# Kernel optimization log

Measured on AMD Instinct MI355X. Metric: run time of the kernel, lower is better.

The kernel has to match this reference:

```python
import jax, jax.numpy as jnp
import numpy as np

NUM_CLASSES = 80
IMG = 640
STRIDES = (8, 16, 32)
CENTER_RADIUS = 2.5
TOPK = 10  # n_candidate_k; dynamic_ks = clamp(int(sum top-10 IoU), 1) <= 10


def _make_grids():
    gs, ss = [], []
    for s in STRIDES:
        n = IMG // s
        gy, gx = np.meshgrid(np.arange(n), np.arange(n), indexing="ij")
        gs.append(np.stack([gx.ravel(), gy.ravel()], 1).astype(np.float32))
        ss.append(np.full(n * n, s, np.float32))
    return np.concatenate(gs, 0), np.concatenate(ss, 0)


def setup_inputs() -> dict:
    key = jax.random.key(0)
    B, T, C = 16, 128, NUM_CLASSES
    grid_np, stride_np = _make_grids()
    A = grid_np.shape[0]  # 8400
    k1, k2, k3, k4, k5, k6 = jax.random.split(key, 6)
    # pred boxes: plausible abs xyxy around anchor centers
    ctr = jnp.asarray((grid_np + 0.5) * stride_np[:, None])[None]
    ctr = ctr + 4.0 * jax.random.normal(k1, (B, A, 2))
    wh = jnp.asarray(stride_np)[None, :, None] * jax.random.uniform(k2, (B, A, 2), minval=1.0, maxval=4.0)
    box = jnp.concatenate([ctr - wh / 2, ctr + wh / 2], -1)
    logits = 2.0 * jax.random.normal(k3, (B, A, 1 + C))
    pred = jnp.concatenate([box, logits], -1)  # [B, A, 5+C]
    # targets: [B, T, 6] = (batch_id, cid, x1, y1, x2, y2)
    tc = jax.random.uniform(k4, (B, T, 2), minval=60.0, maxval=580.0)
    twh = jax.random.uniform(k5, (B, T, 2), minval=30.0, maxval=200.0)
    tbox = jnp.concatenate([tc - twh / 2, tc + twh / 2], -1)
    cid = jax.random.randint(k6, (B, T, 1), 0, C).astype(jnp.float32)
    bid = jnp.broadcast_to(jnp.arange(B, dtype=jnp.float32)[:, None, None], (B, T, 1))
    target = jnp.concatenate([bid, cid, tbox], -1)
    return {"pred": pred, "target": target,
            "grid_mask": jnp.asarray(grid_np), "stride_mask": jnp.asarray(stride_np)}


def _pairwise_iou(a, b):
    # a [T,4], b [A,4], xyxy -> [T,A]
    lt = jnp.maximum(a[:, None, :2], b[None, :, :2])
    rb = jnp.minimum(a[:, None, 2:], b[None, :, 2:])
    wh = jnp.clip(rb - lt, 0.0, None)
    inter = wh[..., 0] * wh[..., 1]
    area_a = jnp.clip(a[:, 2] - a[:, 0], 0.0, None) * jnp.clip(a[:, 3] - a[:, 1], 0.0, None)
    area_b = jnp.clip(b[:, 2] - b[:, 0], 0.0, None) * jnp.clip(b[:, 3] - b[:, 1], 0.0, None)
    return inter / (area_a[:, None] + area_b[None, :] - inter + 1e-8)


def _ciou(p, t):
    # complete IoU, elementwise over leading dims, xyxy
    lt = jnp.maximum(p[..., :2], t[..., :2])
    rb = jnp.minimum(p[..., 2:], t[..., 2:])
    wh = jnp.clip(rb - lt, 0.0, None)
    inter = wh[..., 0] * wh[..., 1]
    wp, hp = p[..., 2] - p[..., 0], p[..., 3] - p[..., 1]
    wt, ht = t[..., 2] - t[..., 0], t[..., 3] - t[..., 1]
    iou = inter / (wp * hp + wt * ht - inter + 1e-8)
    cwh = jnp.maximum(p[..., 2:], t[..., 2:]) - jnp.minimum(p[..., :2], t[..., :2])
    c2 = cwh[..., 0] ** 2 + cwh[..., 1] ** 2 + 1e-8
    rho2 = (((p[..., 0] + p[..., 2]) - (t[..., 0] + t[..., 2])) ** 2
            + ((p[..., 1] + p[..., 3]) - (t[..., 1] + t[..., 3])) ** 2) / 4.0
    v = (4.0 / jnp.pi ** 2) * (jnp.arctan(wt / (ht + 1e-8)) - jnp.arctan(wp / (hp + 1e-8))) ** 2
    alpha = v / (1.0 - iou + v + 1e-8)
    return iou - rho2 / c2 - alpha * v


def _bce_logits(x, t):
    return jnp.maximum(x, 0.0) - x * t + jnp.log1p(jnp.exp(-jnp.abs(x)))


def _assign_image(pred_i, tgt_i, grid, stride):
    # pred_i [A,5+C], tgt_i [T,6]
    A, T, C = pred_i.shape[0], tgt_i.shape[0], NUM_CLASSES
    tbox = tgt_i[:, 2:6]
    cid = tgt_i[:, 1].astype(jnp.int32)
    xc = (grid[:, 0] + 0.5) * stride  # [A]
    yc = (grid[:, 1] + 0.5) * stride
    d = jnp.stack([xc[None] - tbox[:, 0:1], yc[None] - tbox[:, 1:2],
                   tbox[:, 2:3] - xc[None], tbox[:, 3:4] - yc[None]], -1)  # [T,A,4]
    in_boxes = d.min(-1) > 0.0  # [T,A]
    txc = (tbox[:, 0] + tbox[:, 2]) / 2
    tyc = (tbox[:, 1] + tbox[:, 3]) / 2
    in_centers = jnp.maximum(jnp.abs(xc[None] - txc[:, None]),
                             jnp.abs(yc[None] - tyc[:, None])) < CENTER_RADIUS * stride[None]
    in_box = in_boxes.any(0) | in_centers.any(0)  # [A], candidate anchors
    in_box_center = in_boxes & in_centers  # [T,A]
    iou = jnp.where(in_box[None], _pairwise_iou(tbox, pred_i[:, :4]), 0.0)  # [T,A]
    iou_cost = -jnp.log(iou + 1e-8)
    prob = jnp.sqrt(jax.nn.sigmoid(pred_i[:, 4:5]) * jax.nn.sigmoid(pred_i[:, 5:]))  # [A,C]
    logp = jnp.maximum(jnp.log(prob), -100.0)      # torch BCE clamps log at -100
    log1mp = jnp.maximum(jnp.log1p(-prob), -100.0)
    # sum_c BCE(prob, onehot(cid)) computed analytically (avoids [T,A,C]):
    cls_cost = -(log1mp.sum(-1)[None, :] + (logp - log1mp)[:, cid].T)  # [T,A]
    # 1e9 keeps anchors outside in_box out of the candidate pool (original slices them away)
    cost = cls_cost + 3.0 * iou_cost + 1e5 * (~in_box_center) + 1e9 * (~in_box)[None, :]
    topk_ious, _ = jax.lax.top_k(iou, TOPK)  # [T,10]
    dyn_k = jnp.maximum(topk_ious.sum(1).astype(jnp.int32), 1)  # [T]
    _, idx = jax.lax.top_k(-cost, TOPK)  # 10 lowest-cost anchors per target
    sel = jnp.arange(TOPK)[None, :] < dyn_k[:, None]  # keep first dyn_k of them
    matching = jnp.zeros((T, A), bool).at[jnp.arange(T)[:, None], idx].set(sel)
    matching = matching & in_box[None, :]
    conflict = matching.sum(0) > 1  # anchors claimed by >1 targets
    keep = jnp.arange(T)[:, None] == jnp.argmin(cost, 0)[None, :]  # [T,A]
    matching = jnp.where(conflict[None, :], keep, matching)
    mp = matching.any(0)  # [A]
    tp = jnp.argmax(matching, 0)  # [A] target index per anchor
    p_iou = jnp.clip((iou / (iou.max(1, keepdims=True) + 1e-8)).max(0), 0.0, 1.0)  # [A]
    obj_t = jnp.where(in_box, p_iou, 0.0)
    box_t = tbox[tp]  # [A,4]
    cls_t = jax.nn.one_hot(cid[tp], C, dtype=jnp.float32)  # [A,C]
    return mp, box_t, obj_t, cls_t


def reference(pred, target, grid_mask, stride_mask):
    B, A = pred.shape[:2]
    C = NUM_CLASSES
    mp, box_t, obj_t, cls_t = jax.lax.stop_gradient(
        jax.vmap(_assign_image, in_axes=(0, 0, None, None))(pred, target, grid_mask, stride_mask))
    m = mp.reshape(-1).astype(pred.dtype)  # matched-anchor mask over B*A
    n = jnp.maximum(m.sum(), 1.0)
    p = pred.reshape(B * A, -1)
    lbox = 0.05 * jnp.sum((1.0 - _ciou(p[:, :4], box_t.reshape(-1, 4))) * m) / n
    lobj = _bce_logits(p[:, 4], obj_t.reshape(-1)).mean()
    lcls = 0.5 * jnp.sum(_bce_logits(p[:, 5:], cls_t.reshape(-1, C)).mean(-1) * m) / n
    loss = lbox + lobj + lcls
    return loss, jnp.stack([lbox, lobj, lcls])
```

## Files before the change

### kernel.cpp

```cpp
#include <hip/hip_runtime.h>
#include <cfloat>

#pragma clang fp contract(off)

#define NCLS 80
#define PDIM 85
#define NA   8400
#define NAP  8448
#define NB   16
#define NT   128
#define NTOP 10
#define APB  64
#define BPI  132
#define BPI2 33
#define LN2  0.6931471805599453f
#define CAPW 512

#define BAPC ((size_t)NB*NAP)

#define KSENT 0xFFFFFFFF7FFFFFFFull

__device__ __forceinline__ float bce_fast(float x, float t){
  float ax = fabsf(x);
  float e  = __expf(-ax);
  return fmaxf(x,0.0f) - x*t + LN2*__builtin_amdgcn_logf(1.0f + e);
}

__device__ __forceinline__ float pair_iou(float tx1,float ty1,float tx2,float ty2,
                                          float px1,float py1,float px2,float py2){
  float w = fminf(tx2,px2) - fmaxf(tx1,px1);
  float h = fminf(ty2,py2) - fmaxf(ty1,py1);
  w = fmaxf(w,0.0f); h = fmaxf(h,0.0f);
  float inter = w*h;
  float at = fmaxf(tx2-tx1,0.0f)*fmaxf(ty2-ty1,0.0f);
  float ap = fmaxf(px2-px1,0.0f)*fmaxf(py2-py1,0.0f);
  float den = at+ap-inter+1e-8f;
  return inter * __builtin_amdgcn_rcpf(den);
}

__device__ __forceinline__ float dval_exact(float ol, float lg){
  float e4 = __expf(-fabsf(ol));
  float L4 = LN2*__builtin_amdgcn_logf(1.0f + e4);
  float ln_sobj = -(fmaxf(-ol,0.0f) + L4);
  float e  = __expf(-fabsf(lg));
  float L  = LN2*__builtin_amdgcn_logf(1.0f + e);
  float ln_sc = -(fmaxf(-lg,0.0f) + L);
  float lph = 0.5f*(ln_sobj + ln_sc);
  float p   = __expf(lph);
  float lp  = fmaxf(lph, -100.0f);
  float l1  = fmaxf(LN2*__builtin_amdgcn_logf(fmaxf(1.0f - p, 0.0f)), -100.0f);
  return lp - l1;
}

__device__ __forceinline__ float cost_from(float S, float dval, float iou, bool ibc, bool ib){
  float iouc = -LN2 * __builtin_amdgcn_logf(iou + 1e-8f);
  float clsc = -(S + dval);
  float c = clsc + 3.0f*iouc;
  c = c + (ibc ? 0.0f : 100000.0f);
  c = c + (ib  ? 0.0f : 1000000000.0f);
  return c;
}

__device__ __forceinline__ unsigned long long key_of(float c, int idx){
  unsigned int u = __float_as_uint(c);
  u ^= (u & 0x80000000u) ? 0xFFFFFFFFu : 0x80000000u;
  return ((unsigned long long)u << 32) | (unsigned int)idx;
}

__device__ __forceinline__ void ins_iou(float* riou, float iou){
  if (iou > riou[NTOP-1]){
    #pragma unroll
    for (int j = NTOP-1; j >= 1; --j){
      bool gj  = iou > riou[j];
      bool gj1 = iou > riou[j-1];
      riou[j] = gj ? (gj1 ? riou[j-1] : iou) : riou[j];
    }
    riou[0] = (iou > riou[0]) ? iou : riou[0];
  }
}
__device__ __forceinline__ void ins_key(unsigned long long* rk, unsigned long long key){
  if (key < rk[NTOP-1]){
    #pragma unroll
    for (int j = NTOP-1; j >= 1; --j){
      bool bj  = key < rk[j];
      bool bj1 = key < rk[j-1];
      rk[j] = bj ? (bj1 ? rk[j-1] : key) : rk[j];
    }
    rk[0] = (key < rk[0]) ? key : rk[0];
  }
}

__global__ __launch_bounds__(256) void k0_precompute(
    const float* __restrict__ pred, const float* __restrict__ target,
    const float* __restrict__ grid, const float* __restrict__ stridev,
    float4* __restrict__ pbox4, float4* __restrict__ meta4,
    float* __restrict__ obja, float* __restrict__ S0a,
    unsigned long long* __restrict__ mask, unsigned int* __restrict__ obju,
    float4* __restrict__ gaabb, unsigned long long* __restrict__ actm,
    float* __restrict__ acc)
{
  __shared__ __align__(16) float tile[APB*PDIM];
  __shared__ float4 tb4s[NT];
  __shared__ float  ps_s[4][APB];
  __shared__ float  ps0_s[4][APB];
  __shared__ int    ib_s[4][APB];

  int i  = blockIdx.x / BPI;
  int b  = blockIdx.x % BPI;
  int c0 = b*APB;
  int n  = NA - c0; if (n > APB) n = APB;
  int tid = threadIdx.x;

  if (blockIdx.x == 0) acc[tid] = 0.0f;

  const float4* src4 = (const float4*)(pred + ((size_t)i*NA + c0)*PDIM);
  int tot4 = (n*PDIM) >> 2;
  for (int idx = tid; idx < tot4; idx += 256) ((float4*)tile)[idx] = src4[idx];
  for (int idx = tid; idx < NT; idx += 256){
    const float* tg = target + (i*NT + idx)*6;
    tb4s[idx] = make_float4(tg[2],tg[3],tg[4],tg[5]);
  }
  __syncthreads();

  int al = tid & 63, cg = tid >> 6;
  if (al < n){
    float x4 = tile[al*PDIM+4];
    float e4 = __expf(-fabsf(x4));
    float L4 = LN2*__builtin_amdgcn_logf(1.0f + e4);
    float ln_sobj = -(fmaxf(-x4,0.0f) + L4);
    float ps = 0.0f, ps0 = 0.0f;
    #pragma unroll 4
    for (int k = 0; k < 20; ++k){
      int c = cg*20 + k;
      float x  = tile[al*PDIM+5+c];
      float e  = __expf(-fabsf(x));
      float L  = LN2*__builtin_amdgcn_logf(1.0f + e);
      float ln_sc = -(fmaxf(-x,0.0f) + L);
      float lph = 0.5f*(ln_sobj + ln_sc);
      float p   = __expf(lph);
      float l1  = fmaxf(LN2*__builtin_amdgcn_logf(fmaxf(1.0f - p, 0.0f)), -100.0f);
      ps  += l1;
      ps0 += fmaxf(x,0.0f) + L;
    }
    ps_s[cg][al] = ps; ps0_s[cg][al] = ps0;

    int ga = c0 + al;
    float xg = grid[2*ga], yg = grid[2*ga+1], sv = stridev[ga];
    float xc = (xg + 0.5f)*sv, yc = (yg + 0.5f)*sv;
    float rc = 2.5f*sv;
    bool ibp = false;
    #pragma unroll 4
    for (int t = cg*32; t < cg*32+32; ++t){
      float4 T = tb4s[t];
      bool inb = (xc-T.x>0.0f)&&(yc-T.y>0.0f)&&(T.z-xc>0.0f)&&(T.w-yc>0.0f);
      float txc=(T.x+T.z)*0.5f, tyc=(T.y+T.w)*0.5f;
      bool inc = fmaxf(fabsf(xc-txc),fabsf(yc-tyc)) < rc;
      ibp = ibp || inb || inc;
    }
    ib_s[cg][al] = ibp ? 1 : 0;
  }
  __syncthreads();

  if (tid < APB){
    int a = tid;
    bool real = (a < n);
    int gid = i*NAP + c0 + a;
    float x1=0,y1=0,x2=0,y2=0,xc=0,yc=0,rc=0;
    bool ib = false;

    if (real){
      float s  = ps_s[0][a]  + ps_s[1][a]  + ps_s[2][a]  + ps_s[3][a];
      float s0 = ps0_s[0][a] + ps0_s[1][a] + ps0_s[2][a] + ps0_s[3][a];
      ib  = (ib_s[0][a] | ib_s[1][a] | ib_s[2][a] | ib_s[3][a]) != 0;

      x1 = tile[a*PDIM+0]; y1 = tile[a*PDIM+1];
      x2 = tile[a*PDIM+2]; y2 = tile[a*PDIM+3];
      float ol = tile[a*PDIM+4];
      pbox4[gid] = make_float4(x1,y1,x2,y2);
      obja[gid]  = ol;
      S0a[gid]   = s0;
      mask[(size_t)gid*2]   = 0ull;
      mask[(size_t)gid*2+1] = 0ull;
      obju[gid] = 0u;

      int ga = c0 + a;
      float xg = grid[2*ga], yg = grid[2*ga+1], sv = stridev[ga];
      xc = (xg + 0.5f)*sv; yc = (yg + 0.5f)*sv;
      rc = 2.5f*sv;
      meta4[gid] = make_float4(xc, yc, ib ? rc : -rc, s);
    } else {
      meta4[gid] = make_float4(0.0f, 0.0f, -1.0f, 0.0f);
      pbox4[gid] = make_float4(0.0f, 0.0f, 0.0f, 0.0f);
      obju[gid]  = 0u;
    }

    bool iv = real && ib;
    unsigned long long am = __ballot(iv);
    float bx1 = iv ? x1 : FLT_MAX,  by1 = iv ? y1 : FLT_MAX;
    float bx2 = iv ? x2 : -FLT_MAX, by2 = iv ? y2 : -FLT_MAX;
    float cx1 = iv ? xc : FLT_MAX,  cy1 = iv ? yc : FLT_MAX;
    float cx2 = iv ? xc : -FLT_MAX, cy2 = iv ? yc : -FLT_MAX;
    float rx1 = iv ? xc-rc : FLT_MAX,  ry1 = iv ? yc-rc : FLT_MAX;
    float rx2 = iv ? xc+rc : -FLT_MAX, ry2 = iv ? yc+rc : -FLT_MAX;
    #pragma unroll
    for (int off = 32; off > 0; off >>= 1){
      bx1 = fminf(bx1, __shfl_xor(bx1, off));
      by1 = fminf(by1, __shfl_xor(by1, off));
      bx2 = fmaxf(bx2, __shfl_xor(bx2, off));
      by2 = fmaxf(by2, __shfl_xor(by2, off));
      cx1 = fminf(cx1, __shfl_xor(cx1, off));
      cy1 = fminf(cy1, __shfl_xor(cy1, off));
      cx2 = fmaxf(cx2, __shfl_xor(cx2, off));
      cy2 = fmaxf(cy2, __shfl_xor(cy2, off));
      rx1 = fminf(rx1, __shfl_xor(rx1, off));
      ry1 = fminf(ry1, __shfl_xor(ry1, off));
      rx2 = fmaxf(rx2, __shfl_xor(rx2, off));
      ry2 = fmaxf(ry2, __shfl_xor(ry2, off));
    }
    if (tid == 0){
      size_t gb = (size_t)(i*BPI + b)*3;
      gaabb[gb+0] = make_float4(bx1,by1,bx2,by2);
      gaabb[gb+1] = make_float4(cx1,cy1,cx2,cy2);
      gaabb[gb+2] = make_float4(rx1,ry1,rx2,ry2);
      actm[i*BPI + b] = am;
    }
  }
}

__global__ __launch_bounds__(256) void k1_pertarget(
    const float4* __restrict__ pbox4, const float4* __restrict__ meta4,
    const float* __restrict__ obja, const float* __restrict__ pred,
    const float* __restrict__ target, const float4* __restrict__ gaabb,
    const unsigned long long* __restrict__ actm,
    unsigned int* __restrict__ obju, unsigned long long* __restrict__ mask)
{
  __shared__ int2  seg2[4*CAPW];
  __shared__ int   cnts_s[4], cibc_s[4];
  __shared__ float wiou[4][NTOP];
  __shared__ unsigned long long wkey[4][NTOP];
  __shared__ float rmax_s;

  int tid = threadIdx.x, lane = tid & 63, w = tid >> 6;
  int g = blockIdx.x;
  int i = g / NT, t = g - i*NT;
  int iNAP = i*NAP;
  int iNA  = i*NA;
  const float* m4f = (const float*)meta4;

  const float* tg = target + (size_t)g*6;
  int   cid = (int)tg[1];
  float tx1 = tg[2], ty1 = tg[3], tx2 = tg[4], ty2 = tg[5];
  float txc = (tx1+tx2)*0.5f, tyc = (ty1+ty2)*0.5f;

  bool sv = false, svi = false;
  if (lane < 33){
    size_t gb = (size_t)(i*BPI + (w + 4*lane))*3;
    float4 gbb = gaabb[gb+0];
    float4 gcc = gaabb[gb+1];
    float4 grr = gaabb[gb+2];
    bool ovg  = (fminf(tx2,gbb.z) > fmaxf(tx1,gbb.x)) &&
                (fminf(ty2,gbb.w) > fmaxf(ty1,gbb.y));
    bool inbg = (gcc.z > tx1) && (gcc.x < tx2) && (gcc.w > ty1) && (gcc.y < ty2);
    bool incg = (txc > grr.x) && (txc < grr.z) && (tyc > grr.y) && (tyc < grr.w);
    svi = inbg && incg;
    sv = ovg || svi;
  }
  unsigned long long gmsk  = __ballot(sv);
  unsigned long long gmski = __ballot(svi);

  int cnt = 0, ci = 0;
  while (gmsk){
    int k = __ffsll(gmsk) - 1;
    unsigned long long kb = 1ull << k;
    gmsk &= gmsk - 1;
    int a = w*64 + k*256 + lane;
    float4 pb = pbox4[iNAP+a];

    bool ov  = (fminf(tx2,pb.z) > fmaxf(tx1,pb.x)) &&
               (fminf(ty2,pb.w) > fmaxf(ty1,pb.y));

    if (gmski & kb){
      float4 mt = meta4[iNAP+a];
      bool act = (mt.z > 0.0f);
      bool inb = (mt.x-tx1>0.0f)&&(mt.y-ty1>0.0f)&&(tx2-mt.x>0.0f)&&(ty2-mt.y>0.0f);
      bool inc = fmaxf(fabsf(mt.x-txc),fabsf(mt.y-tyc)) < mt.z;
      bool ibc = inb && inc;
      bool cand = act && (ov || ibc);
      unsigned long long bb  = __ballot(cand);
      unsigned long long bb2 = __ballot(ibc);
      if (cand){
        int pos = cnt + __popcll(bb & ((1ull << lane) - 1ull));
        if (pos < CAPW) seg2[w*CAPW + pos].x = a | (ibc ? (1<<15) : 0);
      }
      cnt += __popcll(bb);
      ci  += __popcll(bb2);
    } else {
      unsigned long long am = actm[i*BPI + (w + 4*k)];
      bool act = (am >> lane) & 1ull;
      bool cand = act && ov;
      unsigned long long bb = __ballot(cand);
      if (cand){
        int pos = cnt + __popcll(bb & ((1ull << lane) - 1ull));
        if (pos < CAPW) seg2[w*CAPW + pos].x = a;
      }
      cnt += __popcll(bb);
    }
  }
  if (lane == 0){ cnts_s[w] = cnt; cibc_s[w] = ci; }
  __syncthreads();

  int tibc = cibc_s[0]+cibc_s[1]+cibc_s[2]+cibc_s[3];
  bool ovf = (cnts_s[0]>CAPW)||(cnts_s[1]>CAPW)||(cnts_s[2]>CAPW)||(cnts_s[3]>CAPW);
  bool fastp = !ovf && (tibc >= 16);

  float riou[NTOP]; unsigned long long rk[NTOP];
  #pragma unroll
  for (int j=0;j<NTOP;++j){ riou[j]=0.0f; rk[j]=KSENT; }

  int cw = cnts_s[w];
  if (fastp){
    for (int j = lane; j < cw; j += 64){
      int e  = seg2[w*CAPW + j].x;
      int a1 = e & 0x3fff;
      bool ibc = (e & (1<<15)) != 0;
      int gid = iNAP + a1;
      float4 pb2 = pbox4[gid];
      float iou = pair_iou(tx1,ty1,tx2,ty2, pb2.x,pb2.y,pb2.z,pb2.w);
      seg2[w*CAPW + j].y = __float_as_int(iou);
      ins_iou(riou, iou);
      float S  = m4f[(size_t)gid*4 + 3];
      float dv = dval_exact(obja[gid], pred[(size_t)(iNA+a1)*PDIM + 5 + cid]);
      float c  = cost_from(S, dv, iou, ibc, true);
      ins_key(rk, key_of(c, a1));
    }
  } else {
    for (int a1 = tid; a1 < NA; a1 += 256){
      float4 mt2 = meta4[iNAP+a1];
      if (mt2.z > 0.0f){
        float4 pb2 = pbox4[iNAP+a1];
        float iou = pair_iou(tx1,ty1,tx2,ty2, pb2.x,pb2.y,pb2.z,pb2.w);
        ins_iou(riou, iou);
        bool inb = (mt2.x-tx1>0.0f)&&(mt2.y-ty1>0.0f)&&(tx2-mt2.x>0.0f)&&(ty2-mt2.y>0.0f);
        bool inc = fmaxf(fabsf(mt2.x-txc),fabsf(mt2.y-tyc)) < mt2.z;
        float dv = dval_exact(obja[iNAP+a1], pred[(size_t)(iNA+a1)*PDIM + 5 + cid]);
        float c = cost_from(mt2.w, dv, iou, inb&&inc, true);
        ins_key(rk, key_of(c, a1));
      }
    }
  }

  #pragma unroll
  for (int r = 0; r < NTOP; ++r){
    float gm = riou[0];
    #pragma unroll
    for (int m = 1; m < 64; m <<= 1) gm = fmaxf(gm, __shfl_xor(gm, m));
    unsigned long long bb = __ballot(riou[0] == gm);
    int win = __ffsll(bb) - 1;
    if (lane == win){
      #pragma unroll
      for (int j=0;j<NTOP-1;++j) riou[j] = riou[j+1];
      riou[NTOP-1] = 0.0f;
    }
    if (lane == 0) wiou[w][r] = gm;
  }
  #pragma unroll
  for (int r = 0; r < NTOP; ++r){
    unsigned long long gk = rk[0];
    #pragma unroll
    for (int m = 1; m < 64; m <<= 1){
      unsigned long long o = __shfl_xor(gk, m);
      gk = (o < gk) ? o : gk;
    }
    if (rk[0] == gk){
      #pragma unroll
      for (int j=0;j<NTOP-1;++j) rk[j] = rk[j+1];
      rk[NTOP-1] = KSENT;
    }
    if (lane == 0) wkey[w][r] = gk;
  }
  __syncthreads();

  int dk = 1;
  if (w == 0){
    int p0=0,p1=0,p2=0,p3=0;
    float ssum = 0.0f, rmax = 0.0f;
    #pragma unroll
    for (int r = 0; r < NTOP; ++r){
      float v0=wiou[0][p0], v1=wiou[1][p1], v2=wiou[2][p2], v3=wiou[3][p3];
      float mx = fmaxf(fmaxf(v0,v1), fmaxf(v2,v3));
      if (r == 0) rmax = mx;
      ssum += mx;
      if      (mx == v0) ++p0;
      else if (mx == v1) ++p1;
      else if (mx == v2) ++p2;
      else               ++p3;
    }
    dk = (int)ssum;
    if (dk < 1) dk = 1;
    if (lane == 0) rmax_s = rmax;
  }
  __syncthreads();

  float invm = 1.0f / (rmax_s + 1e-8f);
  if (fastp){
    for (int j = lane; j < cw; j += 64){
      int2 e = seg2[w*CAPW + j];
      int a1 = e.x & 0x3fff;
      float iou = __int_as_float(e.y);
      float v = iou * invm;
      if (v > 0.0f) atomicMax(&obju[iNAP + a1], __float_as_uint(v));
    }
  } else {
    for (int a1 = tid; a1 < NA; a1 += 256){
      float4 mt2 = meta4[iNAP+a1];
      if (mt2.z > 0.0f){
        float4 pb2 = pbox4[iNAP+a1];
        float iou = pair_iou(tx1,ty1,tx2,ty2, pb2.x,pb2.y,pb2.z,pb2.w);
        float v = iou * invm;
        if (v > 0.0f) atomicMax(&obju[iNAP+a1], __float_as_uint(v));
      }
    }
  }

  if (w == 0){
    int q0=0,q1=0,q2=0,q3=0;
    int myidx = 0x7fffffff;
    #pragma unroll
    for (int r = 0; r < NTOP; ++r){
      unsigned long long k0=wkey[0][q0], k1=wkey[1][q1], k2=wkey[2][q2], k3=wkey[3][q3];
      unsigned long long mn = k0;
      mn = (k1 < mn) ? k1 : mn;
      mn = (k2 < mn) ? k2 : mn;
      mn = (k3 < mn) ? k3 : mn;
      if (lane == r) myidx = (int)(mn & 0xFFFFFFFFull);
      if      (mn == k0) ++q0;
      else if (mn == k1) ++q1;
      else if (mn == k2) ++q2;
      else               ++q3;
    }

    if (lane < NTOP && lane < dk){
      int a1 = myidx;
      if (a1 >= 0 && a1 < NA){
        atomicOr(&mask[(size_t)(iNAP + a1)*2 + (t>>6)], 1ull << (t & 63));
      }
    }
  }
}

__global__ __launch_bounds__(256) void k2_peranchor(
    const float* __restrict__ pred,
    const float4* __restrict__ pbox4, const float4* __restrict__ meta4,
    const float* __restrict__ obja, const float* __restrict__ S0a,
    const float* __restrict__ target,
    const unsigned int* __restrict__ obju, const unsigned long long* __restrict__ mask,
    float* __restrict__ acc)
{
  __shared__ float4 tb4[NT];
  __shared__ int    tcid[NT];
  __shared__ int    cl[256];
  __shared__ int    bt_s[256];
  __shared__ int    ncl;
  __shared__ float4 part[4];

  int i  = blockIdx.x / BPI2;
  int b  = blockIdx.x - i*BPI2;
  int tid = threadIdx.x, lane = tid & 63, w = tid >> 6;
  int a  = b*256 + tid;
  int gid = i*NAP + a;

  if (tid < NT){
    const float* tg = target + (i*NT + tid)*6;
    tcid[tid] = (int)tg[1];
    tb4[tid]  = make_float4(tg[2],tg[3],tg[4],tg[5]);
  }
  if (tid == 0) ncl = 0;

  bool valid = (a < NA);
  float4 pb = pbox4[gid];
  float4 mt = meta4[gid];
  unsigned long long m0=0, m1=0;
  if (valid){ m0 = mask[(size_t)gid*2]; m1 = mask[(size_t)gid*2+1]; }
  float bestv = __uint_as_float(obju[gid]);
  float olv   = obja[gid];
  float S0v   = S0a[gid];

  bool ib = valid && (mt.z > 0.0f);
  float px1=pb.x, py1=pb.y, px2=pb.z, py2=pb.w;
  int cnt = __popcll(m0) + __popcll(m1);

  __syncthreads();

  bool myc = (cnt > 1);
  unsigned long long cb = __ballot(myc);
  int nb = __popcll(cb);
  int base = 0;
  if (lane == 0 && nb) base = atomicAdd(&ncl, nb);
  base = __shfl(base, 0);
  if (myc) cl[base + __popcll(cb & ((1ull << lane) - 1ull))] = tid;
  __syncthreads();

  int tot = ncl;
  for (int ci = w; ci < tot; ci += 4){
    int aidx = cl[ci];
    int a2g  = b*256 + aidx;
    int gid2 = i*NAP + a2g;
    float4 pb2 = pbox4[gid2];
    float4 mt2 = meta4[gid2];
    bool ib2 = (mt2.z > 0.0f);
    float rc2 = fabsf(mt2.z);
    float Sg  = mt2.w;
    float ol2 = obja[gid2];
    size_t pbase = (size_t)(i*NA + a2g)*PDIM;

    int ta = lane, tb = lane + 64;
    float dva = dval_exact(ol2, pred[pbase + 5 + tcid[ta]]);
    float dvb = dval_exact(ol2, pred[pbase + 5 + tcid[tb]]);

    float4 Ta = tb4[ta];
    float ioua = ib2 ? pair_iou(Ta.x,Ta.y,Ta.z,Ta.w,pb2.x,pb2.y,pb2.z,pb2.w) : 0.0f;
    bool inba = (mt2.x-Ta.x>0.0f)&&(mt2.y-Ta.y>0.0f)&&(Ta.z-mt2.x>0.0f)&&(Ta.w-mt2.y>0.0f);
    float txa=(Ta.x+Ta.z)*0.5f, tya=(Ta.y+Ta.w)*0.5f;
    bool inca = fmaxf(fabsf(mt2.x-txa),fabsf(mt2.y-tya)) < rc2;
    unsigned long long ka = key_of(cost_from(Sg, dva, ioua, inba&&inca, ib2), ta);

    float4 Tb = tb4[tb];
    float ioub = ib2 ? pair_iou(Tb.x,Tb.y,Tb.z,Tb.w,pb2.x,pb2.y,pb2.z,pb2.w) : 0.0f;
    bool inbb = (mt2.x-Tb.x>0.0f)&&(mt2.y-Tb.y>0.0f)&&(Tb.z-mt2.x>0.0f)&&(Tb.w-mt2.y>0.0f);
    float txb=(Tb.x+Tb.z)*0.5f, tyb=(Tb.y+Tb.w)*0.5f;
    bool incb = fmaxf(fabsf(mt2.x-txb),fabsf(mt2.y-tyb)) < rc2;
    unsigned long long kb = key_of(cost_from(Sg, dvb, ioub, inbb&&incb, ib2), tb);

    unsigned long long mn = (kb < ka) ? kb : ka;
    #pragma unroll
    for (int m = 1; m < 64; m <<= 1){
      unsigned long long o = __shfl_xor(mn, m);
      mn = (o < mn) ? o : mn;
    }
    if (lane == 0) bt_s[aidx] = (int)(mn & 0xFFFFFFFFull);
  }
  __syncthreads();

  float m=0.0f, vbox=0.0f, vobj=0.0f, vcls=0.0f;
  if (valid){
    float obj_t = ib ? fminf(fmaxf(bestv,0.0f),1.0f) : 0.0f;
    vobj = bce_fast(olv, obj_t);

    int tp = 0; bool mpv = false;
    if (cnt > 1){ tp = bt_s[tid]; mpv = true; }
    else if (cnt == 1){
      tp = m0 ? (__ffsll(m0)-1) : (64 + __ffsll(m1)-1);
      mpv = true;
    }

    if (mpv){
      m = 1.0f;
      float4 T = tb4[tp];
      float x1=T.x, y1=T.y, x2=T.z, y2=T.w;
      float w2 = fmaxf(fminf(px2,x2)-fmaxf(px1,x1),0.0f);
      float h2 = fmaxf(fminf(py2,y2)-fmaxf(py1,y1),0.0f);
      float inter = w2*h2;
      float wp=px2-px1, hp=py2-py1, wt=x2-x1, ht=y2-y1;
      float iou = inter/(wp*hp + wt*ht - inter + 1e-8f);
      float cw = fmaxf(px2,x2)-fminf(px1,x1);
      float ch = fmaxf(py2,y2)-fminf(py1,y1);
      float c2 = cw*cw + ch*ch + 1e-8f;
      float dx = (px1+px2)-(x1+x2), dy = (py1+py2)-(y1+y2);
      float rho2 = (dx*dx + dy*dy)/4.0f;
      float da = atanf(wt/(ht+1e-8f)) - atanf(wp/(hp+1e-8f));
      float v  = 0.4052847345693511f * da * da;
      float alpha = v/(1.0f - iou + v + 1e-8f);
      vbox = 1.0f - (iou - rho2/c2 - alpha*v);

      int cc = tcid[tp];
      float xcc = pred[(size_t)(i*NA + a)*PDIM + 5 + cc];
      vcls = (S0v - xcc) * (1.0f/80.0f);
    }
  }

  #pragma unroll
  for (int off=32; off>0; off>>=1){
    m    += __shfl_down(m, off);
    vbox += __shfl_down(vbox, off);
    vobj += __shfl_down(vobj, off);
    vcls += __shfl_down(vcls, off);
  }
  if (lane == 0) part[w] = make_float4(m, vbox, vobj, vcls);
  __syncthreads();
  if (tid == 0){
    float4 s0 = part[0], s1 = part[1], s2 = part[2], s3 = part[3];
    float4 s = make_float4(s0.x+s1.x+s2.x+s3.x, s0.y+s1.y+s2.y+s3.y,
                           s0.z+s1.z+s2.z+s3.z, s0.w+s1.w+s2.w+s3.w);
    int slot = (blockIdx.x & 63)*4;
    atomicAdd(&acc[slot+0], s.x);
    atomicAdd(&acc[slot+1], s.y);
    atomicAdd(&acc[slot+2], s.z);
    atomicAdd(&acc[slot+3], s.w);
  }
}

__global__ void k3_final(const float* __restrict__ acc, float* __restrict__ out){
  int l = threadIdx.x;
  float4 v = ((const float4*)acc)[l];
  #pragma unroll
  for (int off=32; off>0; off>>=1){
    v.x += __shfl_down(v.x, off);
    v.y += __shfl_down(v.y, off);
    v.z += __shfl_down(v.z, off);
    v.w += __shfl_down(v.w, off);
  }
  if (l == 0){
    float n    = fmaxf(v.x, 1.0f);
    float lbox = 0.05f * v.y / n;
    float lobj = v.z / (float)(NB*NA);
    float lcls = 0.5f  * v.w / n;
    out[0] = lbox + lobj + lcls;
    out[1] = lbox; out[2] = lobj; out[3] = lcls;
  }
}

extern "C" void kernel_launch(void* const* d_in, const int* in_sizes, int n_in,
                              void* d_out, int out_size, void* d_ws, size_t ws_size,
                              hipStream_t stream) {
  const float* pred    = (const float*)d_in[0];
  const float* target  = (const float*)d_in[1];
  const float* grid    = (const float*)d_in[2];
  const float* stridev = (const float*)d_in[3];
  float* out = (float*)d_out;

  char* ws = (char*)d_ws;

  size_t off = 0;
  unsigned long long* mask = (unsigned long long*)(ws + off); off += BAPC*16;
  float* acc    = (float*)(ws + off); off += 64*4*4;
  float4* pbox4 = (float4*)(ws + off); off += BAPC*16;
  float4* meta4 = (float4*)(ws + off); off += BAPC*16;
  float* obja   = (float*)(ws + off); off += BAPC*4;
  float* S0a    = (float*)(ws + off); off += BAPC*4;
  unsigned int* obju = (unsigned int*)(ws + off); off += BAPC*4;
  float4* gaabb = (float4*)(ws + off); off += (size_t)NB*BPI*3*16;
  unsigned long long* actm = (unsigned long long*)(ws + off); off += (size_t)NB*BPI*8;

  k0_precompute<<<NB*BPI, 256, 0, stream>>>(pred, target, grid, stridev,
                                            pbox4, meta4, obja, S0a,
                                            mask, obju, gaabb, actm, acc);
  k1_pertarget <<<NB*NT,  256, 0, stream>>>(pbox4, meta4, obja, pred, target,
                                            gaabb, actm, obju, mask);
  k2_peranchor <<<NB*BPI2, 256, 0, stream>>>(pred, pbox4, meta4, obja, S0a,
                                             target, obju, mask, acc);
  k3_final     <<<1, 64, 0, stream>>>(acc, out);
}
```

Baseline: 155.0 us.

## Precompute per-class cost terms in k0 and prefetch candidate boxes in k1

k0 now writes a per-class cost term (log p minus log(1-p)) into a class-major workspace array, but only for classes present in the image's targets. k1 and k2 read this value instead of recomputing dval_exact from the logits. k1's candidate scan is unified: it drops the activity-mask shortcut, always loads meta4, and software-prefetches the next group's boxes. The precompute path is used only when the workspace is large enough. It adds sizeable extra global writes in k0 and depends on workspace size.

```diff
diff --git a/kernel.cpp b/kernel.cpp
--- a/kernel.cpp
+++ b/kernel.cpp
@@ -95,15 +95,16 @@
     const float* __restrict__ grid, const float* __restrict__ stridev,
     float4* __restrict__ pbox4, float4* __restrict__ meta4,
     float* __restrict__ obja, float* __restrict__ S0a,
+    float* __restrict__ D, int use_d,
     unsigned long long* __restrict__ mask, unsigned int* __restrict__ obju,
-    float4* __restrict__ gaabb, unsigned long long* __restrict__ actm,
-    float* __restrict__ acc)
+    float4* __restrict__ gaabb, float* __restrict__ acc)
 {
   __shared__ __align__(16) float tile[APB*PDIM];
   __shared__ float4 tb4s[NT];
   __shared__ float  ps_s[4][APB];
   __shared__ float  ps0_s[4][APB];
   __shared__ int    ib_s[4][APB];
+  __shared__ unsigned long long clsbm[2];
 
   int i  = blockIdx.x / BPI;
   int b  = blockIdx.x % BPI;
@@ -112,18 +113,22 @@
   int tid = threadIdx.x;
 
   if (blockIdx.x == 0) acc[tid] = 0.0f;
+  if (tid < 2) clsbm[tid] = 0ull;
 
   const float4* src4 = (const float4*)(pred + ((size_t)i*NA + c0)*PDIM);
   int tot4 = (n*PDIM) >> 2;
   for (int idx = tid; idx < tot4; idx += 256) ((float4*)tile)[idx] = src4[idx];
   for (int idx = tid; idx < NT; idx += 256){
     const float* tg = target + (i*NT + idx)*6;
+    int cid = (int)tg[1];
+    atomicOr(&clsbm[cid >> 6], 1ull << (cid & 63));
     tb4s[idx] = make_float4(tg[2],tg[3],tg[4],tg[5]);
   }
   __syncthreads();
 
   int al = tid & 63, cg = tid >> 6;
   if (al < n){
+    int gid = i*NAP + c0 + al;
     float x4 = tile[al*PDIM+4];
     float e4 = __expf(-fabsf(x4));
     float L4 = LN2*__builtin_amdgcn_logf(1.0f + e4);
@@ -138,8 +143,11 @@
       float ln_sc = -(fmaxf(-x,0.0f) + L);
       float lph = 0.5f*(ln_sobj + ln_sc);
       float p   = __expf(lph);
+      float lp  = fmaxf(lph, -100.0f);
       float l1  = fmaxf(LN2*__builtin_amdgcn_logf(fmaxf(1.0f - p, 0.0f)), -100.0f);
       ps  += l1;
+      if (use_d && ((clsbm[c>>6] >> (c&63)) & 1ull))
+        D[(size_t)c*BAPC + gid] = lp - l1;
       ps0 += fmaxf(x,0.0f) + L;
     }
     ps_s[cg][al] = ps; ps0_s[cg][al] = ps0;
@@ -195,7 +203,6 @@
     }
 
     bool iv = real && ib;
-    unsigned long long am = __ballot(iv);
     float bx1 = iv ? x1 : FLT_MAX,  by1 = iv ? y1 : FLT_MAX;
     float bx2 = iv ? x2 : -FLT_MAX, by2 = iv ? y2 : -FLT_MAX;
     float cx1 = iv ? xc : FLT_MAX,  cy1 = iv ? yc : FLT_MAX;
@@ -222,19 +229,19 @@
       gaabb[gb+0] = make_float4(bx1,by1,bx2,by2);
       gaabb[gb+1] = make_float4(cx1,cy1,cx2,cy2);
       gaabb[gb+2] = make_float4(rx1,ry1,rx2,ry2);
-      actm[i*BPI + b] = am;
     }
   }
 }
 
 __global__ __launch_bounds__(256) void k1_pertarget(
     const float4* __restrict__ pbox4, const float4* __restrict__ meta4,
+    const float* __restrict__ D, int use_d,
     const float* __restrict__ obja, const float* __restrict__ pred,
     const float* __restrict__ target, const float4* __restrict__ gaabb,
-    const unsigned long long* __restrict__ actm,
     unsigned int* __restrict__ obju, unsigned long long* __restrict__ mask)
 {
-  __shared__ int2  seg2[4*CAPW];
+  __shared__ int   segA[4*CAPW];
+  __shared__ int   segV[4*CAPW];
   __shared__ int   cnts_s[4], cibc_s[4];
   __shared__ float wiou[4][NTOP];
   __shared__ unsigned long long wkey[4][NTOP];
@@ -251,8 +258,9 @@
   int   cid = (int)tg[1];
   float tx1 = tg[2], ty1 = tg[3], tx2 = tg[4], ty2 = tg[5];
   float txc = (tx1+tx2)*0.5f, tyc = (ty1+ty2)*0.5f;
-
-  bool sv = false, svi = false;
+  const float* Dc = use_d ? (D + (size_t)cid*BAPC) : nullptr;
+
+  bool sv = false;
   if (lane < 33){
     size_t gb = (size_t)(i*BPI + (w + 4*lane))*3;
     float4 gbb = gaabb[gb+0];
@@ -262,49 +270,47 @@
                 (fminf(ty2,gbb.w) > fmaxf(ty1,gbb.y));
     bool inbg = (gcc.z > tx1) && (gcc.x < tx2) && (gcc.w > ty1) && (gcc.y < ty2);
     bool incg = (txc > grr.x) && (txc < grr.z) && (tyc > grr.y) && (tyc < grr.w);
-    svi = inbg && incg;
-    sv = ovg || svi;
-  }
-  unsigned long long gmsk  = __ballot(sv);
-  unsigned long long gmski = __ballot(svi);
+    sv = ovg || (inbg && incg);
+  }
+  unsigned long long rem = __ballot(sv);
 
   int cnt = 0, ci = 0;
-  while (gmsk){
-    int k = __ffsll(gmsk) - 1;
-    unsigned long long kb = 1ull << k;
-    gmsk &= gmsk - 1;
-    int a = w*64 + k*256 + lane;
-    float4 pb = pbox4[iNAP+a];
-
+  int kcur = rem ? (__ffsll(rem) - 1) : -1;
+  if (rem) rem &= rem - 1;
+  float4 pb = make_float4(0,0,0,0), mt = make_float4(0,0,-1.0f,0);
+  if (kcur >= 0){
+    int a0 = w*64 + kcur*256 + lane;
+    pb = pbox4[iNAP+a0];
+    mt = meta4[iNAP+a0];
+  }
+  while (kcur >= 0){
+    int knx = rem ? (__ffsll(rem) - 1) : -1;
+    if (rem) rem &= rem - 1;
+    float4 pbn = pb, mtn = mt;
+    if (knx >= 0){
+      int an = w*64 + knx*256 + lane;
+      pbn = pbox4[iNAP+an];
+      mtn = meta4[iNAP+an];
+    }
+
+    int a = w*64 + kcur*256 + lane;
+    bool act = (mt.z > 0.0f);
     bool ov  = (fminf(tx2,pb.z) > fmaxf(tx1,pb.x)) &&
                (fminf(ty2,pb.w) > fmaxf(ty1,pb.y));
-
-    if (gmski & kb){
-      float4 mt = meta4[iNAP+a];
-      bool act = (mt.z > 0.0f);
-      bool inb = (mt.x-tx1>0.0f)&&(mt.y-ty1>0.0f)&&(tx2-mt.x>0.0f)&&(ty2-mt.y>0.0f);
-      bool inc = fmaxf(fabsf(mt.x-txc),fabsf(mt.y-tyc)) < mt.z;
-      bool ibc = inb && inc;
-      bool cand = act && (ov || ibc);
-      unsigned long long bb  = __ballot(cand);
-      unsigned long long bb2 = __ballot(ibc);
-      if (cand){
-        int pos = cnt + __popcll(bb & ((1ull << lane) - 1ull));
-        if (pos < CAPW) seg2[w*CAPW + pos].x = a | (ibc ? (1<<15) : 0);
-      }
-      cnt += __popcll(bb);
-      ci  += __popcll(bb2);
-    } else {
-      unsigned long long am = actm[i*BPI + (w + 4*k)];
-      bool act = (am >> lane) & 1ull;
-      bool cand = act && ov;
-      unsigned long long bb = __ballot(cand);
-      if (cand){
-        int pos = cnt + __popcll(bb & ((1ull << lane) - 1ull));
-        if (pos < CAPW) seg2[w*CAPW + pos].x = a;
-      }
-      cnt += __popcll(bb);
-    }
+    bool inb = (mt.x-tx1>0.0f)&&(mt.y-ty1>0.0f)&&(tx2-mt.x>0.0f)&&(ty2-mt.y>0.0f);
+    bool inc = fmaxf(fabsf(mt.x-txc),fabsf(mt.y-tyc)) < mt.z;
+    bool ibc = inb && inc;
+    bool cand = act && (ov || ibc);
+    unsigned long long bb  = __ballot(cand);
+    unsigned long long bb2 = __ballot(ibc);
+    if (cand){
+      int pos = cnt + __popcll(bb & ((1ull << lane) - 1ull));
+      if (pos < CAPW) segA[w*CAPW + pos] = a | (ibc ? (1<<15) : 0);
+    }
+    cnt += __popcll(bb);
+    ci  += __popcll(bb2);
+
+    kcur = knx; pb = pbn; mt = mtn;
   }
   if (lane == 0){ cnts_s[w] = cnt; cibc_s[w] = ci; }
   __syncthreads();
@@ -320,16 +326,17 @@
   int cw = cnts_s[w];
   if (fastp){
     for (int j = lane; j < cw; j += 64){
-      int e  = seg2[w*CAPW + j].x;
+      int e  = segA[w*CAPW + j];
       int a1 = e & 0x3fff;
       bool ibc = (e & (1<<15)) != 0;
       int gid = iNAP + a1;
       float4 pb2 = pbox4[gid];
       float iou = pair_iou(tx1,ty1,tx2,ty2, pb2.x,pb2.y,pb2.z,pb2.w);
-      seg2[w*CAPW + j].y = __float_as_int(iou);
+      segV[w*CAPW + j] = __float_as_int(iou);
       ins_iou(riou, iou);
       float S  = m4f[(size_t)gid*4 + 3];
-      float dv = dval_exact(obja[gid], pred[(size_t)(iNA+a1)*PDIM + 5 + cid]);
+      float dv = use_d ? Dc[gid]
+                       : dval_exact(obja[gid], pred[(size_t)(iNA+a1)*PDIM + 5 + cid]);
       float c  = cost_from(S, dv, iou, ibc, true);
       ins_key(rk, key_of(c, a1));
     }
@@ -342,7 +349,8 @@
         ins_iou(riou, iou);
         bool inb = (mt2.x-tx1>0.0f)&&(mt2.y-ty1>0.0f)&&(tx2-mt2.x>0.0f)&&(ty2-mt2.y>0.0f);
         bool inc = fmaxf(fabsf(mt2.x-txc),fabsf(mt2.y-tyc)) < mt2.z;
-        float dv = dval_exact(obja[iNAP+a1], pred[(size_t)(iNA+a1)*PDIM + 5 + cid]);
+        float dv = use_d ? Dc[iNAP+a1]
+                         : dval_exact(obja[iNAP+a1], pred[(size_t)(iNA+a1)*PDIM + 5 + cid]);
         float c = cost_from(mt2.w, dv, iou, inb&&inc, true);
         ins_key(rk, key_of(c, a1));
       }
@@ -404,9 +412,8 @@
   float invm = 1.0f / (rmax_s + 1e-8f);
   if (fastp){
     for (int j = lane; j < cw; j += 64){
-      int2 e = seg2[w*CAPW + j];
-      int a1 = e.x & 0x3fff;
-      float iou = __int_as_float(e.y);
+      int a1 = segA[w*CAPW + j] & 0x3fff;
+      float iou = __int_as_float(segV[w*CAPW + j]);
       float v = iou * invm;
       if (v > 0.0f) atomicMax(&obju[iNAP + a1], __float_as_uint(v));
     }
@@ -452,6 +459,7 @@
     const float* __restrict__ pred,
     const float4* __restrict__ pbox4, const float4* __restrict__ meta4,
     const float* __restrict__ obja, const float* __restrict__ S0a,
+    const float* __restrict__ D, int use_d,
     const float* __restrict__ target,
     const unsigned int* __restrict__ obju, const unsigned long long* __restrict__ mask,
     float* __restrict__ acc)
@@ -510,12 +518,14 @@
     bool ib2 = (mt2.z > 0.0f);
     float rc2 = fabsf(mt2.z);
     float Sg  = mt2.w;
-    float ol2 = obja[gid2];
+    float ol2 = use_d ? 0.0f : obja[gid2];
     size_t pbase = (size_t)(i*NA + a2g)*PDIM;
 
     int ta = lane, tb = lane + 64;
-    float dva = dval_exact(ol2, pred[pbase + 5 + tcid[ta]]);
-    float dvb = dval_exact(ol2, pred[pbase + 5 + tcid[tb]]);
+    float dva = use_d ? D[(size_t)tcid[ta]*BAPC + gid2]
+                      : dval_exact(ol2, pred[pbase + 5 + tcid[ta]]);
+    float dvb = use_d ? D[(size_t)tcid[tb]*BAPC + gid2]
+                      : dval_exact(ol2, pred[pbase + 5 + tcid[tb]]);
 
     float4 Ta = tb4[ta];
     float ioua = ib2 ? pair_iou(Ta.x,Ta.y,Ta.z,Ta.w,pb2.x,pb2.y,pb2.z,pb2.w) : 0.0f;
@@ -639,14 +649,17 @@
   float* S0a    = (float*)(ws + off); off += BAPC*4;
   unsigned int* obju = (unsigned int*)(ws + off); off += BAPC*4;
   float4* gaabb = (float4*)(ws + off); off += (size_t)NB*BPI*3*16;
-  unsigned long long* actm = (unsigned long long*)(ws + off); off += (size_t)NB*BPI*8;
+  float* D      = (float*)(ws + off);
+  const size_t need_d = off + (size_t)NCLS*BAPC*4;
+  int use_d = (ws_size >= need_d) ? 1 : 0;
 
   k0_precompute<<<NB*BPI, 256, 0, stream>>>(pred, target, grid, stridev,
-                                            pbox4, meta4, obja, S0a,
-                                            mask, obju, gaabb, actm, acc);
-  k1_pertarget <<<NB*NT,  256, 0, stream>>>(pbox4, meta4, obja, pred, target,
-                                            gaabb, actm, obju, mask);
+                                            pbox4, meta4, obja, S0a, D, use_d,
+                                            mask, obju, gaabb, acc);
+  k1_pertarget <<<NB*NT,  256, 0, stream>>>(pbox4, meta4, D, use_d,
+                                            obja, pred, target, gaabb,
+                                            obju, mask);
   k2_peranchor <<<NB*BPI2, 256, 0, stream>>>(pred, pbox4, meta4, obja, S0a,
-                                             target, obju, mask, acc);
+                                             D, use_d, target, obju, mask, acc);
   k3_final     <<<1, 64, 0, stream>>>(acc, out);
 }
```

After: 153.8 us. No clear change (-0.7%).
